# Performance work log

Measured on AMD Instinct MI355X. Metric: run time of the kernel, lower is better.

The kernel has to match this reference:

```python
import jax, jax.numpy as jnp
import numpy as np

D_MODEL = 128
N_HEADS = 4
D_K = D_V = 32
LN_EPS = 1e-5


def setup_inputs() -> dict:
    key = jax.random.key(0)
    ks = jax.random.split(key, 12)
    B, S = 8, 2048
    scale = 1.0 / np.sqrt(D_MODEL)
    inp = {
        "Q": jax.random.normal(ks[0], (B, S, D_MODEL), jnp.float32),
        "K": jax.random.normal(ks[1], (B, S, D_MODEL), jnp.float32),
        "V": jax.random.normal(ks[2], (B, S, D_MODEL), jnp.float32),
        "attn_mask": jnp.zeros((B, S, S), jnp.bool_),
        # learned params (torch Linear stored as [in, out] so y = x @ W + b)
        "wq": jax.random.normal(ks[3], (D_MODEL, N_HEADS * D_K), jnp.float32) * scale,
        "bq": jnp.zeros((N_HEADS * D_K,), jnp.float32),
        "wk": jax.random.normal(ks[4], (D_MODEL, N_HEADS * D_K), jnp.float32) * scale,
        "bk": jnp.zeros((N_HEADS * D_K,), jnp.float32),
        "wv": jax.random.normal(ks[5], (D_MODEL, N_HEADS * D_V), jnp.float32) * scale,
        "bv": jnp.zeros((N_HEADS * D_V,), jnp.float32),
        "wo": jax.random.normal(ks[6], (N_HEADS * D_V, D_MODEL), jnp.float32) * scale,
        "bo": jnp.zeros((D_MODEL,), jnp.float32),
        "gamma": jnp.ones((D_MODEL,), jnp.float32),
        "beta": jnp.zeros((D_MODEL,), jnp.float32),
    }
    return inp


def _layer_norm(x, gamma, beta):
    mu = jnp.mean(x, axis=-1, keepdims=True)
    var = jnp.mean(jnp.square(x - mu), axis=-1, keepdims=True)
    return (x - mu) * jax.lax.rsqrt(var + LN_EPS) * gamma + beta


def reference(Q, K, V, attn_mask, wq, bq, wk, bk, wv, bv, wo, bo, gamma, beta):
    B, S, _ = Q.shape
    residual = Q
    # project and split heads: [B, H, S, Dk]
    q = (Q @ wq + bq).reshape(B, S, N_HEADS, D_K).transpose(0, 2, 1, 3)
    k = (K @ wk + bk).reshape(B, S, N_HEADS, D_K).transpose(0, 2, 1, 3)
    v = (V @ wv + bv).reshape(B, S, N_HEADS, D_V).transpose(0, 2, 1, 3)
    scores = jnp.einsum("bhqd,bhkd->bhqk", q, k) / np.sqrt(D_K)
    scores = jnp.where(attn_mask[:, None, :, :], -1e9, scores)
    attn = jax.nn.softmax(scores, axis=-1)
    context = jnp.einsum("bhqk,bhkd->bhqd", attn, v)
    context = context.transpose(0, 2, 1, 3).reshape(B, S, N_HEADS * D_V)
    output = context @ wo + bo
    out = _layer_norm(output + residual, gamma, beta)
    return out, attn
```

## Files before the change

kernel.cpp:

```cpp
#include <hip/hip_runtime.h>

typedef _Float16 f16;
typedef __attribute__((ext_vector_type(8))) _Float16 f16x8;
typedef __attribute__((ext_vector_type(4))) _Float16 f16x4;
typedef __attribute__((ext_vector_type(2))) __fp16 fp16x2;
typedef __attribute__((ext_vector_type(4))) float f32x4;
typedef unsigned int u32;
typedef __attribute__((ext_vector_type(2))) unsigned int u32x2;
typedef __attribute__((ext_vector_type(4))) unsigned int u32x4;

#define S_LEN 2048
#define NB 8
#define NH 4
#define DM 128
#define DK 32

static __device__ __forceinline__ f32x4 mfma_16x16x32(f16x8 a, f16x8 b, f32x4 c) {
  return __builtin_amdgcn_mfma_f32_16x16x32_f16(a, b, c, 0, 0, 0);
}
static __device__ __forceinline__ float exp2f_fast(float x) {
  return __builtin_amdgcn_exp2f(x);
}

union H8 { f16x8 v; fp16x2 h[4]; };
union H4 { f16x4 v; fp16x2 h[2]; };

__global__ __launch_bounds__(256) void wtrans_kernel(
    const float* __restrict__ wq, const float* __restrict__ wk,
    const float* __restrict__ wv, const float* __restrict__ wo,
    f16* __restrict__ wt)
{
  const float* W = (blockIdx.x == 0) ? wq : (blockIdx.x == 1) ? wk
                 : (blockIdx.x == 2) ? wv : wo;
  f16* dst = wt + (size_t)blockIdx.x * 16384;
  __shared__ f16 tile[128 * 130];
  const int t = threadIdx.x;
#pragma unroll
  for (int i = 0; i < 16; ++i) {
    int idx = (i * 256 + t) * 4;
    f32x4 w4 = *(const f32x4*)(W + idx);
    int k = idx >> 7, j = idx & 127;
    tile[(j    ) * 130 + k] = (f16)w4[0];
    tile[(j + 1) * 130 + k] = (f16)w4[1];
    tile[(j + 2) * 130 + k] = (f16)w4[2];
    tile[(j + 3) * 130 + k] = (f16)w4[3];
  }
  __syncthreads();
#pragma unroll
  for (int i = 0; i < 8; ++i) {
    int lin = (i * 256 + t) * 8;
    int j = lin >> 7, k = lin & 127;
    f16x8 v;
#pragma unroll
    for (int r = 0; r < 8; ++r) v[r] = tile[j * 130 + k + r];
    *(f16x8*)(dst + lin) = v;
  }
}

__global__ __launch_bounds__(256, 2) void proj_pack_kernel(
    const float* __restrict__ Qx, const float* __restrict__ Kx, const float* __restrict__ Vx,
    const f16* __restrict__ wt,
    const float* __restrict__ bq, const float* __restrict__ bk, const float* __restrict__ bv,
    f16* __restrict__ qh, f16* __restrict__ kh, f16* __restrict__ vt,
    const unsigned char* __restrict__ mask, u32* __restrict__ words)
{
  const int bx = blockIdx.x;
  if (bx >= 768) {
    const size_t tid = (size_t)(bx - 768) * 256 + threadIdx.x;
    const unsigned char* src = mask + tid * 64;
    u32 w0 = 0, w1 = 0;
#pragma unroll
    for (int wi = 0; wi < 2; ++wi) {
      u32x4 a = *(const u32x4*)(src + wi * 32);
      u32x4 c = *(const u32x4*)(src + wi * 32 + 16);
      u32 bits = 0;
#pragma unroll
      for (int i = 0; i < 4; ++i) {
        u32 ua = a[i], uc = c[i];
#pragma unroll
        for (int k = 0; k < 4; ++k) {
          bits |= (((ua >> (8 * k)) & 0xffu) ? 1u : 0u) << (4 * i + k);
          bits |= (((uc >> (8 * k)) & 0xffu) ? 1u : 0u) << (16 + 4 * i + k);
        }
      }
      if (wi == 0) w0 = bits; else w1 = bits;
    }
    u32x2 o; o[0] = w0; o[1] = w1;
    *(u32x2*)(words + tid * 2) = o;
    return;
  }

  const int mode = bx >> 8;
  const int bxx = bx & 255;
  const float* X = (mode == 0) ? Qx : (mode == 1) ? Kx : Vx;
  const f16* wm = wt + (size_t)mode * 16384;
  const float* Bp = (mode == 0) ? bq : (mode == 1) ? bk : bv;

  const int wave = threadIdx.x >> 6, lane = threadIdx.x & 63;
  const int ln = lane & 15, hi = lane >> 4;
  const int rows0 = bxx * 64 + wave * 16;
  const int b = rows0 >> 11;
  const int s0 = rows0 & (S_LEN - 1);

  const float* xp = X + (size_t)(rows0 + ln) * DM + hi * 8;
  H8 hx[4];
#pragma unroll
  for (int kc = 0; kc < 4; ++kc) {
    f32x4 x0 = *(const f32x4*)(xp + kc * 32);
    f32x4 x1 = *(const f32x4*)(xp + kc * 32 + 4);
    hx[kc].h[0] = __builtin_amdgcn_cvt_pkrtz(x0[0], x0[1]);
    hx[kc].h[1] = __builtin_amdgcn_cvt_pkrtz(x0[2], x0[3]);
    hx[kc].h[2] = __builtin_amdgcn_cvt_pkrtz(x1[0], x1[1]);
    hx[kc].h[3] = __builtin_amdgcn_cvt_pkrtz(x1[2], x1[3]);
  }

  f32x4 acc[8];
#pragma unroll
  for (int jg = 0; jg < 8; ++jg) acc[jg] = (f32x4){0.f, 0.f, 0.f, 0.f};

  const f16* wp = wm + ln * 128 + hi * 8;
  f16x8 wf[8];
#pragma unroll
  for (int jg = 0; jg < 8; ++jg) wf[jg] = *(const f16x8*)(wp + jg * 2048);
#pragma unroll
  for (int kc = 0; kc < 4; ++kc) {
    f16x8 nwf[8];
    if (kc < 3) {
#pragma unroll
      for (int jg = 0; jg < 8; ++jg)
        nwf[jg] = *(const f16x8*)(wp + jg * 2048 + (kc + 1) * 32);
    }
    if (mode < 2) {
#pragma unroll
      for (int jg = 0; jg < 8; ++jg) acc[jg] = mfma_16x16x32(wf[jg], hx[kc].v, acc[jg]);
    } else {
#pragma unroll
      for (int jg = 0; jg < 8; ++jg) acc[jg] = mfma_16x16x32(hx[kc].v, wf[jg], acc[jg]);
    }
#pragma unroll
    for (int jg = 0; jg < 8; ++jg) wf[jg] = nwf[jg];
  }

  if (mode < 2) {
    const float sc = (mode == 0) ? 0.25503531f : 1.0f;
    f16* outp = (mode == 0) ? qh : kh;
    const int s = s0 + ln;
#pragma unroll
    for (int jg = 0; jg < 8; ++jg) {
      int j0 = jg * 16 + hi * 4;
      f32x4 bb = *(const f32x4*)(Bp + j0);
      int h = jg >> 1;
      int dd0 = (jg & 1) * 16 + hi * 4;
      f16x4 e;
#pragma unroll
      for (int r = 0; r < 4; ++r) e[r] = (f16)((acc[jg][r] + bb[r]) * sc);
      *(f16x4*)(outp + ((size_t)(b * NH + h) * S_LEN + s) * DK + dd0) = e;
    }
  } else {
    const int t4 = s0 >> 5;
    const int halfq = (s0 >> 4) & 1;
#pragma unroll
    for (int jt = 0; jt < 8; ++jt) {
      int h = jt >> 1;
      int dv = (jt & 1) * 16 + ln;
      float bb = Bp[jt * 16 + ln];
      H4 u;
      u.h[0] = __builtin_amdgcn_cvt_pkrtz(acc[jt][0] + bb, acc[jt][1] + bb);
      u.h[1] = __builtin_amdgcn_cvt_pkrtz(acc[jt][2] + bb, acc[jt][3] + bb);
      f16* dst = vt + (size_t)(b * NH + h) * DK * S_LEN + t4 * 1024 + dv * 32 + hi * 8 + halfq * 4;
      *(f16x4*)dst = u.v;
    }
  }
}

__global__ __launch_bounds__(512, 4) void attn_kernel(
    const f16* __restrict__ qh, const f16* __restrict__ kh, const f16* __restrict__ vt,
    const u32* __restrict__ words,
    float* __restrict__ attn, float* __restrict__ ctx)
{
  const int lg = (blockIdx.x & 7) * 256 + (blockIdx.x >> 3);
  const int bh = lg >> 6;
  const int qp = lg & 63;
  const int wave = threadIdx.x >> 6;
  const int lane = threadIdx.x & 63;
  const int ln = lane & 15, hi = lane >> 4;
  const int b = bh >> 2, h = bh & 3;
  const int base = qp * 32;
  const int rA = base + ln;
  const int rB = rA + 16;
  const int kv0 = wave * (S_LEN / 8);

  __shared__ f32x4 pt[8][2][16][16];
  __shared__ float sums[8][2][16];

  const f16* kbase = kh + (size_t)bh * S_LEN * DK;
  const f16* vbase = vt + (size_t)bh * DK * S_LEN;
  const u32* wrA = words + ((size_t)b * S_LEN + rA) * (S_LEN / 32);
  const u32* wrB = words + ((size_t)b * S_LEN + rB) * (S_LEN / 32);

  const f16x8 qA = *(const f16x8*)(qh + ((size_t)bh * S_LEN + rA) * DK + hi * 8);
  const f16x8 qB = *(const f16x8*)(qh + ((size_t)bh * S_LEN + rB) * DK + hi * 8);
  const f32x4 zero = {0.f, 0.f, 0.f, 0.f};

  float smA = 0.f, smB = 0.f;
  {
    const f16* kp = kbase + (size_t)(kv0 + ln) * DK + hi * 8;
    const u32* mpA = wrA + (kv0 >> 5);
    const u32* mpB = wrB + (kv0 >> 5);
    f16x8 k0 = *(const f16x8*)(kp);
    f16x8 k1 = *(const f16x8*)(kp + 512);
    f16x8 k2 = *(const f16x8*)(kp + 1024);
    f16x8 k3 = *(const f16x8*)(kp + 1536);
    u32x2 mA = *(const u32x2*)mpA;
    u32x2 mB = *(const u32x2*)mpB;
    for (int it = 0; it < 4; ++it) {
      f16x8 n0, n1, n2, n3;
      u32x2 nA, nB;
      if (it < 3) {
        n0 = *(const f16x8*)(kp + 2048);
        n1 = *(const f16x8*)(kp + 2560);
        n2 = *(const f16x8*)(kp + 3072);
        n3 = *(const f16x8*)(kp + 3584);
        nA = *(const u32x2*)(mpA + 2);
        nB = *(const u32x2*)(mpB + 2);
      }
      f32x4 sA0 = mfma_16x16x32(k0, qA, zero);
      f32x4 sA1 = mfma_16x16x32(k1, qA, zero);
      f32x4 sA2 = mfma_16x16x32(k2, qA, zero);
      f32x4 sA3 = mfma_16x16x32(k3, qA, zero);
      f32x4 sB0 = mfma_16x16x32(k0, qB, zero);
      f32x4 sB1 = mfma_16x16x32(k1, qB, zero);
      f32x4 sB2 = mfma_16x16x32(k2, qB, zero);
      f32x4 sB3 = mfma_16x16x32(k3, qB, zero);
      if (__any(((mA[0] | mA[1]) | (mB[0] | mB[1])) != 0u)) {
#pragma unroll
        for (int r = 0; r < 4; ++r) {
          float a0 = ((mA[0] >> (4 * hi + r)) & 1) ? 0.f : exp2f_fast(sA0[r]);
          float a1 = ((mA[0] >> (16 + 4 * hi + r)) & 1) ? 0.f : exp2f_fast(sA1[r]);
          float a2 = ((mA[1] >> (4 * hi + r)) & 1) ? 0.f : exp2f_fast(sA2[r]);
          float a3 = ((mA[1] >> (16 + 4 * hi + r)) & 1) ? 0.f : exp2f_fast(sA3[r]);
          smA += (a0 + a1) + (a2 + a3);
          float b0 = ((mB[0] >> (4 * hi + r)) & 1) ? 0.f : exp2f_fast(sB0[r]);
          float b1 = ((mB[0] >> (16 + 4 * hi + r)) & 1) ? 0.f : exp2f_fast(sB1[r]);
          float b2 = ((mB[1] >> (4 * hi + r)) & 1) ? 0.f : exp2f_fast(sB2[r]);
          float b3 = ((mB[1] >> (16 + 4 * hi + r)) & 1) ? 0.f : exp2f_fast(sB3[r]);
          smB += (b0 + b1) + (b2 + b3);
        }
      } else {
#pragma unroll
        for (int r = 0; r < 4; ++r) {
          smA += (exp2f_fast(sA0[r]) + exp2f_fast(sA1[r])) + (exp2f_fast(sA2[r]) + exp2f_fast(sA3[r]));
          smB += (exp2f_fast(sB0[r]) + exp2f_fast(sB1[r])) + (exp2f_fast(sB2[r]) + exp2f_fast(sB3[r]));
        }
      }
      k0 = n0; k1 = n1; k2 = n2; k3 = n3;
      mA = nA; mB = nB;
      kp += 2048; mpA += 2; mpB += 2;
    }
  }
  smA += __shfl_xor(smA, 16); smA += __shfl_xor(smA, 32);
  smB += __shfl_xor(smB, 16); smB += __shfl_xor(smB, 32);
  if (lane < 16) { sums[wave][0][ln] = smA; sums[wave][1][ln] = smB; }
  __syncthreads();
  const float linvA = -__builtin_amdgcn_logf(
      ((sums[0][0][ln] + sums[1][0][ln]) + (sums[2][0][ln] + sums[3][0][ln])) +
      ((sums[4][0][ln] + sums[5][0][ln]) + (sums[6][0][ln] + sums[7][0][ln])));
  const float linvB = -__builtin_amdgcn_logf(
      ((sums[0][1][ln] + sums[1][1][ln]) + (sums[2][1][ln] + sums[3][1][ln])) +
      ((sums[4][1][ln] + sums[5][1][ln]) + (sums[6][1][ln] + sums[7][1][ln])));

  f32x4 cA0 = zero, cA1 = zero, cB0 = zero, cB1 = zero;
  {
    const f16* kp = kbase + (size_t)(kv0 + ln) * DK + hi * 8;
    const f16* vp = vbase + (size_t)(kv0 >> 5) * 1024 + ln * 32 + hi * 8;
    const u32* mpA = wrA + (kv0 >> 5);
    const u32* mpB = wrB + (kv0 >> 5);
    float* dstA = attn + ((size_t)bh * S_LEN + base) * S_LEN + kv0;
    float* dstB = dstA + (size_t)16 * S_LEN;
    f16x8 k0 = *(const f16x8*)(kp);
    f16x8 k1 = *(const f16x8*)(kp + 512);
    f16x8 k2 = *(const f16x8*)(kp + 1024);
    f16x8 k3 = *(const f16x8*)(kp + 1536);
    for (int it = 0; it < 4; ++it) {
      f16x8 v0 = *(const f16x8*)(vp);
      f16x8 v1 = *(const f16x8*)(vp + 512);
      f16x8 v2 = *(const f16x8*)(vp + 1024);
      f16x8 v3 = *(const f16x8*)(vp + 1536);
      f16x8 n0, n1, n2, n3;
      if (it < 3) {
        n0 = *(const f16x8*)(kp + 2048);
        n1 = *(const f16x8*)(kp + 2560);
        n2 = *(const f16x8*)(kp + 3072);
        n3 = *(const f16x8*)(kp + 3584);
      }
      u32x2 mA = *(const u32x2*)mpA;
      u32x2 mB = *(const u32x2*)mpB;

      {
        f32x4 s0 = mfma_16x16x32(k0, qA, zero);
        f32x4 s1 = mfma_16x16x32(k1, qA, zero);
        f32x4 s2 = mfma_16x16x32(k2, qA, zero);
        f32x4 s3 = mfma_16x16x32(k3, qA, zero);
        f32x4 p0, p1, p2, p3;
        if (__any((mA[0] | mA[1]) != 0u)) {
#pragma unroll
          for (int r = 0; r < 4; ++r) {
            p0[r] = ((mA[0] >> (4 * hi + r)) & 1) ? 0.f : exp2f_fast(s0[r] + linvA);
            p1[r] = ((mA[0] >> (16 + 4 * hi + r)) & 1) ? 0.f : exp2f_fast(s1[r] + linvA);
            p2[r] = ((mA[1] >> (4 * hi + r)) & 1) ? 0.f : exp2f_fast(s2[r] + linvA);
            p3[r] = ((mA[1] >> (16 + 4 * hi + r)) & 1) ? 0.f : exp2f_fast(s3[r] + linvA);
          }
        } else {
#pragma unroll
          for (int r = 0; r < 4; ++r) {
            p0[r] = exp2f_fast(s0[r] + linvA);
            p1[r] = exp2f_fast(s1[r] + linvA);
            p2[r] = exp2f_fast(s2[r] + linvA);
            p3[r] = exp2f_fast(s3[r] + linvA);
          }
        }
        pt[wave][0][ln][(0 + hi) ^ (ln & 7)] = p0;
        pt[wave][0][ln][(4 + hi) ^ (ln & 7)] = p1;
        pt[wave][0][ln][(8 + hi) ^ (ln & 7)] = p2;
        pt[wave][0][ln][(12 + hi) ^ (ln & 7)] = p3;
        H8 ua, ub;
        ua.h[0] = __builtin_amdgcn_cvt_pkrtz(p0[0], p0[1]);
        ua.h[1] = __builtin_amdgcn_cvt_pkrtz(p0[2], p0[3]);
        ua.h[2] = __builtin_amdgcn_cvt_pkrtz(p1[0], p1[1]);
        ua.h[3] = __builtin_amdgcn_cvt_pkrtz(p1[2], p1[3]);
        ub.h[0] = __builtin_amdgcn_cvt_pkrtz(p2[0], p2[1]);
        ub.h[1] = __builtin_amdgcn_cvt_pkrtz(p2[2], p2[3]);
        ub.h[2] = __builtin_amdgcn_cvt_pkrtz(p3[0], p3[1]);
        ub.h[3] = __builtin_amdgcn_cvt_pkrtz(p3[2], p3[3]);
        cA0 = mfma_16x16x32(v0, ua.v, cA0);
        cA1 = mfma_16x16x32(v1, ua.v, cA1);
        cA0 = mfma_16x16x32(v2, ub.v, cA0);
        cA1 = mfma_16x16x32(v3, ub.v, cA1);
#pragma unroll
        for (int s4 = 0; s4 < 4; ++s4) {
          int row = s4 * 4 + hi;
          f32x4 val = pt[wave][0][row][ln ^ (row & 7)];
          __builtin_nontemporal_store(val, (f32x4*)(dstA + (size_t)row * S_LEN + ln * 4));
        }
      }
      {
        f32x4 s0 = mfma_16x16x32(k0, qB, zero);
        f32x4 s1 = mfma_16x16x32(k1, qB, zero);
        f32x4 s2 = mfma_16x16x32(k2, qB, zero);
        f32x4 s3 = mfma_16x16x32(k3, qB, zero);
        f32x4 p0, p1, p2, p3;
        if (__any((mB[0] | mB[1]) != 0u)) {
#pragma unroll
          for (int r = 0; r < 4; ++r) {
            p0[r] = ((mB[0] >> (4 * hi + r)) & 1) ? 0.f : exp2f_fast(s0[r] + linvB);
            p1[r] = ((mB[0] >> (16 + 4 * hi + r)) & 1) ? 0.f : exp2f_fast(s1[r] + linvB);
            p2[r] = ((mB[1] >> (4 * hi + r)) & 1) ? 0.f : exp2f_fast(s2[r] + linvB);
            p3[r] = ((mB[1] >> (16 + 4 * hi + r)) & 1) ? 0.f : exp2f_fast(s3[r] + linvB);
          }
        } else {
#pragma unroll
          for (int r = 0; r < 4; ++r) {
            p0[r] = exp2f_fast(s0[r] + linvB);
            p1[r] = exp2f_fast(s1[r] + linvB);
            p2[r] = exp2f_fast(s2[r] + linvB);
            p3[r] = exp2f_fast(s3[r] + linvB);
          }
        }
        pt[wave][1][ln][(0 + hi) ^ (ln & 7)] = p0;
        pt[wave][1][ln][(4 + hi) ^ (ln & 7)] = p1;
        pt[wave][1][ln][(8 + hi) ^ (ln & 7)] = p2;
        pt[wave][1][ln][(12 + hi) ^ (ln & 7)] = p3;
        H8 ua, ub;
        ua.h[0] = __builtin_amdgcn_cvt_pkrtz(p0[0], p0[1]);
        ua.h[1] = __builtin_amdgcn_cvt_pkrtz(p0[2], p0[3]);
        ua.h[2] = __builtin_amdgcn_cvt_pkrtz(p1[0], p1[1]);
        ua.h[3] = __builtin_amdgcn_cvt_pkrtz(p1[2], p1[3]);
        ub.h[0] = __builtin_amdgcn_cvt_pkrtz(p2[0], p2[1]);
        ub.h[1] = __builtin_amdgcn_cvt_pkrtz(p2[2], p2[3]);
        ub.h[2] = __builtin_amdgcn_cvt_pkrtz(p3[0], p3[1]);
        ub.h[3] = __builtin_amdgcn_cvt_pkrtz(p3[2], p3[3]);
        cB0 = mfma_16x16x32(v0, ua.v, cB0);
        cB1 = mfma_16x16x32(v1, ua.v, cB1);
        cB0 = mfma_16x16x32(v2, ub.v, cB0);
        cB1 = mfma_16x16x32(v3, ub.v, cB1);
#pragma unroll
        for (int s4 = 0; s4 < 4; ++s4) {
          int row = s4 * 4 + hi;
          f32x4 val = pt[wave][1][row][ln ^ (row & 7)];
          __builtin_nontemporal_store(val, (f32x4*)(dstB + (size_t)row * S_LEN + ln * 4));
        }
      }
      k0 = n0; k1 = n1; k2 = n2; k3 = n3;
      kp += 2048; vp += 2048; mpA += 2; mpB += 2;
      dstA += 64; dstB += 64;
    }
  }

  if (wave != 0) {
    float* cb = (float*)&pt[wave][0][0][0];
#pragma unroll
    for (int r = 0; r < 4; ++r) {
      cb[ln * 32 + hi * 4 + r] = cA0[r];
      cb[ln * 32 + 16 + hi * 4 + r] = cA1[r];
      cb[(16 + ln) * 32 + hi * 4 + r] = cB0[r];
      cb[(16 + ln) * 32 + 16 + hi * 4 + r] = cB1[r];
    }
  }
  __syncthreads();
  if (wave == 0) {
#pragma unroll
    for (int w = 1; w < 8; ++w) {
      const float* cb = (const float*)&pt[w][0][0][0];
#pragma unroll
      for (int r = 0; r < 4; ++r) {
        cA0[r] += cb[ln * 32 + hi * 4 + r];
        cA1[r] += cb[ln * 32 + 16 + hi * 4 + r];
        cB0[r] += cb[(16 + ln) * 32 + hi * 4 + r];
        cB1[r] += cb[(16 + ln) * 32 + 16 + hi * 4 + r];
      }
    }
    float* crowA = ctx + ((size_t)b * S_LEN + rA) * DM + h * DK;
    float* crowB = ctx + ((size_t)b * S_LEN + rB) * DM + h * DK;
    *(f32x4*)(crowA + hi * 4) = cA0;
    *(f32x4*)(crowA + 16 + hi * 4) = cA1;
    *(f32x4*)(crowB + hi * 4) = cB0;
    *(f32x4*)(crowB + 16 + hi * 4) = cB1;
  }
}

__global__ __launch_bounds__(256, 2) void out_ln_kernel(
    const float* __restrict__ ctx, const float* __restrict__ Qin,
    const f16* __restrict__ wt,
    const float* __restrict__ bo,
    const float* __restrict__ gamma, const float* __restrict__ beta,
    float* __restrict__ out)
{
  const f16* wm = wt + (size_t)3 * 16384;
  const int wave = threadIdx.x >> 6, lane = threadIdx.x & 63;
  const int ln = lane & 15, hi = lane >> 4;
  const int srow = blockIdx.x * 64 + wave * 16 + ln;

  const float* xp = ctx + (size_t)srow * DM + hi * 8;
  H8 hx[4];
#pragma unroll
  for (int kc = 0; kc < 4; ++kc) {
    f32x4 x0 = *(const f32x4*)(xp + kc * 32);
    f32x4 x1 = *(const f32x4*)(xp + kc * 32 + 4);
    hx[kc].h[0] = __builtin_amdgcn_cvt_pkrtz(x0[0], x0[1]);
    hx[kc].h[1] = __builtin_amdgcn_cvt_pkrtz(x0[2], x0[3]);
    hx[kc].h[2] = __builtin_amdgcn_cvt_pkrtz(x1[0], x1[1]);
    hx[kc].h[3] = __builtin_amdgcn_cvt_pkrtz(x1[2], x1[3]);
  }

  f32x4 acc[8];
#pragma unroll
  for (int jg = 0; jg < 8; ++jg) acc[jg] = (f32x4){0.f, 0.f, 0.f, 0.f};

  const f16* wp = wm + ln * 128 + hi * 8;
  f16x8 wf[8];
#pragma unroll
  for (int jg = 0; jg < 8; ++jg) wf[jg] = *(const f16x8*)(wp + jg * 2048);
#pragma unroll
  for (int kc = 0; kc < 4; ++kc) {
    f16x8 nwf[8];
    if (kc < 3) {
#pragma unroll
      for (int jg = 0; jg < 8; ++jg)
        nwf[jg] = *(const f16x8*)(wp + jg * 2048 + (kc + 1) * 32);
    }
#pragma unroll
    for (int jg = 0; jg < 8; ++jg) acc[jg] = mfma_16x16x32(wf[jg], hx[kc].v, acc[jg]);
#pragma unroll
    for (int jg = 0; jg < 8; ++jg) wf[jg] = nwf[jg];
  }

  float sm = 0.f, sq = 0.f;
#pragma unroll
  for (int jg = 0; jg < 8; ++jg) {
    int j0 = jg * 16 + hi * 4;
    f32x4 bb = *(const f32x4*)(bo + j0);
    f32x4 qq = *(const f32x4*)(Qin + (size_t)srow * DM + j0);
#pragma unroll
    for (int r = 0; r < 4; ++r) {
      float y = acc[jg][r] + bb[r] + qq[r];
      acc[jg][r] = y;
      sm += y; sq += y * y;
    }
  }
  sm += __shfl_xor(sm, 16); sm += __shfl_xor(sm, 32);
  sq += __shfl_xor(sq, 16); sq += __shfl_xor(sq, 32);
  const float mu = sm * (1.f / 128.f);
  const float var = sq * (1.f / 128.f) - mu * mu;
  const float rstd = rsqrtf(var + 1e-5f);
#pragma unroll
  for (int jg = 0; jg < 8; ++jg) {
    int j0 = jg * 16 + hi * 4;
    f32x4 g = *(const f32x4*)(gamma + j0);
    f32x4 be = *(const f32x4*)(beta + j0);
    f32x4 o;
#pragma unroll
    for (int r = 0; r < 4; ++r) o[r] = (acc[jg][r] - mu) * rstd * g[r] + be[r];
    *(f32x4*)(out + (size_t)srow * DM + j0) = o;
  }
}

extern "C" void kernel_launch(void* const* d_in, const int* in_sizes, int n_in,
                              void* d_out, int out_size, void* d_ws, size_t ws_size,
                              hipStream_t stream) {
  const float* Q    = (const float*)d_in[0];
  const float* K    = (const float*)d_in[1];
  const float* V    = (const float*)d_in[2];
  const unsigned char* mask = (const unsigned char*)d_in[3];
  const float* wq   = (const float*)d_in[4];
  const float* bq   = (const float*)d_in[5];
  const float* wk   = (const float*)d_in[6];
  const float* bk   = (const float*)d_in[7];
  const float* wv   = (const float*)d_in[8];
  const float* bv   = (const float*)d_in[9];
  const float* wo   = (const float*)d_in[10];
  const float* bo   = (const float*)d_in[11];
  const float* gamma= (const float*)d_in[12];
  const float* beta = (const float*)d_in[13];

  const size_t HEAD_ELEMS = (size_t)NB * NH * S_LEN * DK;

  f16* qh = (f16*)d_ws;
  f16* kh = qh + HEAD_ELEMS;
  f16* vt = kh + HEAD_ELEMS;
  float* ctx = (float*)(vt + HEAD_ELEMS);
  u32* words = (u32*)(ctx + (size_t)NB * S_LEN * DM);
  f16* wt = (f16*)(words + (size_t)NB * S_LEN * (S_LEN / 32));

  float* out  = (float*)d_out;
  float* attn = out + (size_t)NB * S_LEN * DM;

  wtrans_kernel<<<4, 256, 0, stream>>>(wq, wk, wv, wo, wt);
  proj_pack_kernel<<<2816, 256, 0, stream>>>(Q, K, V, wt, bq, bk, bv, qh, kh, vt, mask, words);
  attn_kernel<<<2048, 512, 0, stream>>>(qh, kh, vt, words, attn, ctx);
  out_ln_kernel<<<256, 256, 0, stream>>>(ctx, Q, wt, bo, gamma, beta, out);
}
```

Measured before the change: 160.7 us.

## Fuse output projection and LayerNorm into attention kernel via last-block counter

Removes the separate out_ln kernel launch. Each attention block bumps an atomic counter per (batch, 32-row query group) after writing its context slice. The fourth block to arrive, the one that completes all heads, runs the output projection, residual add and LayerNorm for those 32 rows using two waves. This saves a kernel launch and its tail, but adds a memset launch, a threadfence plus atomic, and serial epilogue work at the end of some attention blocks. It also drops the weight-prefetch double buffering.

```diff
diff --git a/kernel.cpp b/kernel.cpp
--- a/kernel.cpp
+++ b/kernel.cpp
@@ -176,7 +176,11 @@
 __global__ __launch_bounds__(512, 4) void attn_kernel(
     const f16* __restrict__ qh, const f16* __restrict__ kh, const f16* __restrict__ vt,
     const u32* __restrict__ words,
-    float* __restrict__ attn, float* __restrict__ ctx)
+    float* __restrict__ attn, float* __restrict__ ctx,
+    const f16* __restrict__ wt, const float* __restrict__ bo,
+    const float* __restrict__ gamma, const float* __restrict__ beta,
+    const float* __restrict__ Qin, float* __restrict__ out,
+    u32* __restrict__ cnt)
 {
   const int lg = (blockIdx.x & 7) * 256 + (blockIdx.x >> 3);
   const int bh = lg >> 6;
@@ -192,6 +196,7 @@
 
   __shared__ f32x4 pt[8][2][16][16];
   __shared__ float sums[8][2][16];
+  __shared__ int lnflag;
 
   const f16* kbase = kh + (size_t)bh * S_LEN * DK;
   const f16* vbase = vt + (size_t)bh * DK * S_LEN;
@@ -261,6 +266,7 @@
   smA += __shfl_xor(smA, 16); smA += __shfl_xor(smA, 32);
   smB += __shfl_xor(smB, 16); smB += __shfl_xor(smB, 32);
   if (lane < 16) { sums[wave][0][ln] = smA; sums[wave][1][ln] = smB; }
+  if (threadIdx.x == 0) lnflag = 0;
   __syncthreads();
   const float linvA = -__builtin_amdgcn_logf(
       ((sums[0][0][ln] + sums[1][0][ln]) + (sums[2][0][ln] + sums[3][0][ln])) +
@@ -425,82 +431,73 @@
     *(f32x4*)(crowA + 16 + hi * 4) = cA1;
     *(f32x4*)(crowB + hi * 4) = cB0;
     *(f32x4*)(crowB + 16 + hi * 4) = cB1;
-  }
-}
-
-__global__ __launch_bounds__(256, 2) void out_ln_kernel(
-    const float* __restrict__ ctx, const float* __restrict__ Qin,
-    const f16* __restrict__ wt,
-    const float* __restrict__ bo,
-    const float* __restrict__ gamma, const float* __restrict__ beta,
-    float* __restrict__ out)
-{
-  const f16* wm = wt + (size_t)3 * 16384;
-  const int wave = threadIdx.x >> 6, lane = threadIdx.x & 63;
-  const int ln = lane & 15, hi = lane >> 4;
-  const int srow = blockIdx.x * 64 + wave * 16 + ln;
-
-  const float* xp = ctx + (size_t)srow * DM + hi * 8;
-  H8 hx[4];
-#pragma unroll
-  for (int kc = 0; kc < 4; ++kc) {
-    f32x4 x0 = *(const f32x4*)(xp + kc * 32);
-    f32x4 x1 = *(const f32x4*)(xp + kc * 32 + 4);
-    hx[kc].h[0] = __builtin_amdgcn_cvt_pkrtz(x0[0], x0[1]);
-    hx[kc].h[1] = __builtin_amdgcn_cvt_pkrtz(x0[2], x0[3]);
-    hx[kc].h[2] = __builtin_amdgcn_cvt_pkrtz(x1[0], x1[1]);
-    hx[kc].h[3] = __builtin_amdgcn_cvt_pkrtz(x1[2], x1[3]);
-  }
-
-  f32x4 acc[8];
-#pragma unroll
-  for (int jg = 0; jg < 8; ++jg) acc[jg] = (f32x4){0.f, 0.f, 0.f, 0.f};
-
-  const f16* wp = wm + ln * 128 + hi * 8;
-  f16x8 wf[8];
-#pragma unroll
-  for (int jg = 0; jg < 8; ++jg) wf[jg] = *(const f16x8*)(wp + jg * 2048);
-#pragma unroll
-  for (int kc = 0; kc < 4; ++kc) {
-    f16x8 nwf[8];
-    if (kc < 3) {
-#pragma unroll
-      for (int jg = 0; jg < 8; ++jg)
-        nwf[jg] = *(const f16x8*)(wp + jg * 2048 + (kc + 1) * 32);
-    }
-#pragma unroll
-    for (int jg = 0; jg < 8; ++jg) acc[jg] = mfma_16x16x32(wf[jg], hx[kc].v, acc[jg]);
-#pragma unroll
-    for (int jg = 0; jg < 8; ++jg) wf[jg] = nwf[jg];
-  }
-
-  float sm = 0.f, sq = 0.f;
-#pragma unroll
-  for (int jg = 0; jg < 8; ++jg) {
-    int j0 = jg * 16 + hi * 4;
-    f32x4 bb = *(const f32x4*)(bo + j0);
-    f32x4 qq = *(const f32x4*)(Qin + (size_t)srow * DM + j0);
-#pragma unroll
-    for (int r = 0; r < 4; ++r) {
-      float y = acc[jg][r] + bb[r] + qq[r];
-      acc[jg][r] = y;
-      sm += y; sq += y * y;
-    }
-  }
-  sm += __shfl_xor(sm, 16); sm += __shfl_xor(sm, 32);
-  sq += __shfl_xor(sq, 16); sq += __shfl_xor(sq, 32);
-  const float mu = sm * (1.f / 128.f);
-  const float var = sq * (1.f / 128.f) - mu * mu;
-  const float rstd = rsqrtf(var + 1e-5f);
-#pragma unroll
-  for (int jg = 0; jg < 8; ++jg) {
-    int j0 = jg * 16 + hi * 4;
-    f32x4 g = *(const f32x4*)(gamma + j0);
-    f32x4 be = *(const f32x4*)(beta + j0);
-    f32x4 o;
-#pragma unroll
-    for (int r = 0; r < 4; ++r) o[r] = (acc[jg][r] - mu) * rstd * g[r] + be[r];
-    *(f32x4*)(out + (size_t)srow * DM + j0) = o;
+    __threadfence();
+    if (lane == 0) {
+      u32 old = atomicAdd(&cnt[(b << 6) + qp], 1u);
+      if (old == 3u) lnflag = 1;
+    }
+  }
+  __syncthreads();
+  if (lnflag == 0 || wave >= 2) return;
+
+  {
+    const f16* wm = wt + (size_t)3 * 16384;
+    const size_t srow = (size_t)b * S_LEN + base + wave * 16 + ln;
+
+    const float* xp = ctx + srow * DM + hi * 8;
+    H8 hx[4];
+#pragma unroll
+    for (int kc = 0; kc < 4; ++kc) {
+      f32x4 x0 = *(const f32x4*)(xp + kc * 32);
+      f32x4 x1 = *(const f32x4*)(xp + kc * 32 + 4);
+      hx[kc].h[0] = __builtin_amdgcn_cvt_pkrtz(x0[0], x0[1]);
+      hx[kc].h[1] = __builtin_amdgcn_cvt_pkrtz(x0[2], x0[3]);
+      hx[kc].h[2] = __builtin_amdgcn_cvt_pkrtz(x1[0], x1[1]);
+      hx[kc].h[3] = __builtin_amdgcn_cvt_pkrtz(x1[2], x1[3]);
+    }
+
+    f32x4 acc[8];
+#pragma unroll
+    for (int jg = 0; jg < 8; ++jg) acc[jg] = (f32x4){0.f, 0.f, 0.f, 0.f};
+
+    const f16* wp = wm + ln * 128 + hi * 8;
+#pragma unroll
+    for (int kc = 0; kc < 4; ++kc) {
+#pragma unroll
+      for (int jg = 0; jg < 8; ++jg) {
+        f16x8 wf = *(const f16x8*)(wp + jg * 2048 + kc * 32);
+        acc[jg] = mfma_16x16x32(wf, hx[kc].v, acc[jg]);
+      }
+    }
+
+    float sm = 0.f, sq = 0.f;
+#pragma unroll
+    for (int jg = 0; jg < 8; ++jg) {
+      int j0 = jg * 16 + hi * 4;
+      f32x4 bb = *(const f32x4*)(bo + j0);
+      f32x4 qq = *(const f32x4*)(Qin + srow * DM + j0);
+#pragma unroll
+      for (int r = 0; r < 4; ++r) {
+        float y = acc[jg][r] + bb[r] + qq[r];
+        acc[jg][r] = y;
+        sm += y; sq += y * y;
+      }
+    }
+    sm += __shfl_xor(sm, 16); sm += __shfl_xor(sm, 32);
+    sq += __shfl_xor(sq, 16); sq += __shfl_xor(sq, 32);
+    const float mu = sm * (1.f / 128.f);
+    const float var = sq * (1.f / 128.f) - mu * mu;
+    const float rstd = rsqrtf(var + 1e-5f);
+#pragma unroll
+    for (int jg = 0; jg < 8; ++jg) {
+      int j0 = jg * 16 + hi * 4;
+      f32x4 g = *(const f32x4*)(gamma + j0);
+      f32x4 be = *(const f32x4*)(beta + j0);
+      f32x4 o;
+#pragma unroll
+      for (int r = 0; r < 4; ++r) o[r] = (acc[jg][r] - mu) * rstd * g[r] + be[r];
+      *(f32x4*)(out + srow * DM + j0) = o;
+    }
   }
 }
 
@@ -530,12 +527,14 @@
   float* ctx = (float*)(vt + HEAD_ELEMS);
   u32* words = (u32*)(ctx + (size_t)NB * S_LEN * DM);
   f16* wt = (f16*)(words + (size_t)NB * S_LEN * (S_LEN / 32));
+  u32* cnt = (u32*)(wt + 4 * 16384);
 
   float* out  = (float*)d_out;
   float* attn = out + (size_t)NB * S_LEN * DM;
 
+  hipMemsetAsync(cnt, 0, NB * 64 * sizeof(u32), stream);
   wtrans_kernel<<<4, 256, 0, stream>>>(wq, wk, wv, wo, wt);
   proj_pack_kernel<<<2816, 256, 0, stream>>>(Q, K, V, wt, bq, bk, bv, qh, kh, vt, mask, words);
-  attn_kernel<<<2048, 512, 0, stream>>>(qh, kh, vt, words, attn, ctx);
-  out_ln_kernel<<<256, 256, 0, stream>>>(ctx, Q, wt, bo, gamma, beta, out);
+  attn_kernel<<<2048, 512, 0, stream>>>(qh, kh, vt, words, attn, ctx,
+                                        wt, bo, gamma, beta, Q, out, cnt);
 }
```

Measured after the change: 237.3 us. +47.7%, slower.

## Split output projection K dimension across waves and reduce through shared memory

Applied to the files above, without the earlier changes.

The output-projection plus layernorm kernel now covers 32 rows per block instead of 64. Pairs of waves each handle half of the 128-wide reduction dimension, and the partial sums are combined through LDS after a block barrier. The grid doubles to 512 blocks to raise parallelism and shorten each wave's serial MFMA chain. In exchange it adds a shared-memory round trip and a __syncthreads, and half the waves go idle during the layernorm phase.

```diff
diff --git a/kernel.cpp b/kernel.cpp
--- a/kernel.cpp
+++ b/kernel.cpp
@@ -438,12 +438,16 @@
   const f16* wm = wt + (size_t)3 * 16384;
   const int wave = threadIdx.x >> 6, lane = threadIdx.x & 63;
   const int ln = lane & 15, hi = lane >> 4;
-  const int srow = blockIdx.x * 64 + wave * 16 + ln;
-
-  const float* xp = ctx + (size_t)srow * DM + hi * 8;
-  H8 hx[4];
-#pragma unroll
-  for (int kc = 0; kc < 4; ++kc) {
+  const int rowgrp = wave & 1;
+  const int ksel = wave >> 1;
+  const size_t srow = (size_t)blockIdx.x * 32 + rowgrp * 16 + ln;
+
+  __shared__ float part[2][64][32];
+
+  const float* xp = ctx + srow * DM + ksel * 64 + hi * 8;
+  H8 hx[2];
+#pragma unroll
+  for (int kc = 0; kc < 2; ++kc) {
     f32x4 x0 = *(const f32x4*)(xp + kc * 32);
     f32x4 x1 = *(const f32x4*)(xp + kc * 32 + 4);
     hx[kc].h[0] = __builtin_amdgcn_cvt_pkrtz(x0[0], x0[1]);
@@ -456,22 +460,28 @@
 #pragma unroll
   for (int jg = 0; jg < 8; ++jg) acc[jg] = (f32x4){0.f, 0.f, 0.f, 0.f};
 
-  const f16* wp = wm + ln * 128 + hi * 8;
-  f16x8 wf[8];
-#pragma unroll
-  for (int jg = 0; jg < 8; ++jg) wf[jg] = *(const f16x8*)(wp + jg * 2048);
-#pragma unroll
-  for (int kc = 0; kc < 4; ++kc) {
-    f16x8 nwf[8];
-    if (kc < 3) {
-#pragma unroll
-      for (int jg = 0; jg < 8; ++jg)
-        nwf[jg] = *(const f16x8*)(wp + jg * 2048 + (kc + 1) * 32);
-    }
-#pragma unroll
-    for (int jg = 0; jg < 8; ++jg) acc[jg] = mfma_16x16x32(wf[jg], hx[kc].v, acc[jg]);
-#pragma unroll
-    for (int jg = 0; jg < 8; ++jg) wf[jg] = nwf[jg];
+  const f16* wp = wm + ln * 128 + ksel * 64 + hi * 8;
+#pragma unroll
+  for (int kc = 0; kc < 2; ++kc) {
+#pragma unroll
+    for (int jg = 0; jg < 8; ++jg) {
+      f16x8 wf = *(const f16x8*)(wp + jg * 2048 + kc * 32);
+      acc[jg] = mfma_16x16x32(wf, hx[kc].v, acc[jg]);
+    }
+  }
+
+  if (ksel == 1) {
+#pragma unroll
+    for (int jg = 0; jg < 8; ++jg)
+      *(f32x4*)&part[rowgrp][lane][jg * 4] = acc[jg];
+  }
+  __syncthreads();
+  if (ksel == 1) return;
+#pragma unroll
+  for (int jg = 0; jg < 8; ++jg) {
+    f32x4 p = *(const f32x4*)&part[rowgrp][lane][jg * 4];
+#pragma unroll
+    for (int r = 0; r < 4; ++r) acc[jg][r] += p[r];
   }
 
   float sm = 0.f, sq = 0.f;
@@ -479,7 +489,7 @@
   for (int jg = 0; jg < 8; ++jg) {
     int j0 = jg * 16 + hi * 4;
     f32x4 bb = *(const f32x4*)(bo + j0);
-    f32x4 qq = *(const f32x4*)(Qin + (size_t)srow * DM + j0);
+    f32x4 qq = *(const f32x4*)(Qin + srow * DM + j0);
 #pragma unroll
     for (int r = 0; r < 4; ++r) {
       float y = acc[jg][r] + bb[r] + qq[r];
@@ -500,7 +510,7 @@
     f32x4 o;
 #pragma unroll
     for (int r = 0; r < 4; ++r) o[r] = (acc[jg][r] - mu) * rstd * g[r] + be[r];
-    *(f32x4*)(out + (size_t)srow * DM + j0) = o;
+    *(f32x4*)(out + srow * DM + j0) = o;
   }
 }
 
@@ -537,5 +547,5 @@
   wtrans_kernel<<<4, 256, 0, stream>>>(wq, wk, wv, wo, wt);
   proj_pack_kernel<<<2816, 256, 0, stream>>>(Q, K, V, wt, bq, bk, bv, qh, kh, vt, mask, words);
   attn_kernel<<<2048, 512, 0, stream>>>(qh, kh, vt, words, attn, ctx);
-  out_ln_kernel<<<256, 256, 0, stream>>>(ctx, Q, wt, bo, gamma, beta, out);
-}
+  out_ln_kernel<<<512, 256, 0, stream>>>(ctx, Q, wt, bo, gamma, beta, out);
+}
```

Result: no change. 162.0 us (+0.8%).
